# Kernel tuning notes

Measured on AMD Instinct MI355X. Metric: run time of the kernel, lower is better.

Reference implementation:

```python
import jax, jax.numpy as jnp
import numpy as np

N_NODES = 100000
N_EDGES = 1600000
DIMS = [128, 128, 40]   # embedding_dim
SS_DIM = 64
DROP_P = 0.2


def setup_inputs() -> dict:
    key = jax.random.key(0)
    ks = jax.random.split(key, 8)
    x = jax.random.normal(ks[0], (N_NODES, DIMS[0]), dtype=jnp.float32)
    adj_row = jax.random.randint(ks[1], (N_EDGES,), 0, N_NODES)
    adj_col = jax.random.randint(ks[2], (N_EDGES,), 0, N_NODES)
    adj_val = jax.random.uniform(ks[3], (N_EDGES,), dtype=jnp.float32)
    # nn.Linear(in, out, bias=False): y = x @ W.T; store transposed as (in, out)
    def lin(k, fi, fo):
        b = 1.0 / np.sqrt(fi)
        return jax.random.uniform(k, (fi, fo), minval=-b, maxval=b, dtype=jnp.float32)
    W0 = lin(ks[4], DIMS[0], DIMS[1])
    W1 = lin(ks[5], DIMS[1], DIMS[2])
    Wss = lin(ks[6], DIMS[-2], SS_DIM)
    return {"x": x, "adj_row": adj_row, "adj_col": adj_col, "adj_val": adj_val,
            "W0": W0, "W1": W1, "Wss": Wss}


def reference(x, adj_row, adj_col, adj_val, W0, W1, Wss):
    N = x.shape[0]
    keep = 1.0 - DROP_P

    def spmm(h):  # sparse [N,N] @ dense [N,d] via gather + segment_sum
        return jax.ops.segment_sum(adj_val[:, None] * h[adj_col], adj_row,
                                   num_segments=N)

    # deterministic dropout masks (fixed key, training path val_test=False)
    k1, k2 = jax.random.split(jax.random.key(42))
    m1 = jax.random.bernoulli(k1, keep, (N, W0.shape[1]))
    m2 = jax.random.bernoulli(k2, keep, (N, W0.shape[1]))

    # main branch: ln=0 -> spmm, lin0, relu, dropout; ln=1 -> spmm, lin1
    h = jnp.where(m1, jax.nn.relu(spmm(x) @ W0) / keep, 0.0)
    h = spmm(h) @ W1

    # self-supervised branch: ln=0 -> spmm, lin0, relu, dropout; ln=1 -> spmm; classifier
    s = jnp.where(m2, jax.nn.relu(spmm(x) @ W0) / keep, 0.0)
    s = spmm(s) @ Wss
    return (h, s)
```

## Files before the change

### kernel.cpp

```cpp
#include <hip/hip_runtime.h>
#include <stdint.h>


#define NN 100000
#define NE 1600000
#define D 128
#define NW 400000
#define ZC 104
#define DO1 40
#define DO2 64
#define OUT_S_OFF 4000000
#define KEEP_THR 6710886u
#define NB 49
#define CAP 36000
#define MASKB 3125
#define CONVB 25000

typedef unsigned int uint;
typedef __attribute__((ext_vector_type(4))) float f32x4;
typedef __attribute__((ext_vector_type(8))) short short8;
union U4S8 { uint4 u; short8 s; };

__device__ __forceinline__ float bflo(uint p) { return __uint_as_float(p << 16); }
__device__ __forceinline__ float bfhi(uint p) { return __uint_as_float(p & 0xffff0000u); }
__device__ __forceinline__ uint f2bf(float f) {
  uint u = __float_as_uint(f);
  return (u + 0x7fffu + ((u >> 16) & 1u)) >> 16;
}
__device__ __forceinline__ uint pack2(float lo, float hi) {
  return f2bf(lo) | (f2bf(hi) << 16);
}

__device__ __forceinline__ void tf2x32(uint k0, uint k1, uint x0, uint x1,
                                       uint& o0, uint& o1) {
  uint ks2 = k0 ^ k1 ^ 0x1BD11BDAu;
  x0 += k0; x1 += k1;
#define TFR(r) { x0 += x1; x1 = (x1 << (r)) | (x1 >> (32 - (r))); x1 ^= x0; }
  TFR(13) TFR(15) TFR(26) TFR(6)
  x0 += k1;  x1 += ks2 + 1u;
  TFR(17) TFR(29) TFR(16) TFR(24)
  x0 += ks2; x1 += k0 + 2u;
  TFR(13) TFR(15) TFR(26) TFR(6)
  x0 += k0;  x1 += k1 + 3u;
  TFR(17) TFR(29) TFR(16) TFR(24)
  x0 += k1;  x1 += ks2 + 4u;
  TFR(13) TFR(15) TFR(26) TFR(6)
  x0 += ks2; x1 += k0 + 5u;
#undef TFR
  o0 = x0; o1 = x1;
}

__global__ void prep_kernel(const float* __restrict__ x, uint* __restrict__ xb,
                            uint* __restrict__ m1, uint* __restrict__ m2,
                            const float* __restrict__ W0, const float* __restrict__ W1,
                            const float* __restrict__ Wss,
                            ushort* __restrict__ w0t, ushort* __restrict__ wcatT,
                            int* __restrict__ cursor) {
  int bid = blockIdx.x, tid = threadIdx.x;
  if (bid < CONVB) {
    if (bid == 0 && tid < NB) cursor[tid] = tid * CAP;
    int i = bid * 256 + tid;
    float2 v = ((const float2*)x)[i];
    xb[i] = pack2(v.x, v.y);
  } else if (bid < CONVB + MASKB) {
    int t = (bid - CONVB) * 256 + tid;
    uint a0, a1, b0, b1;
    tf2x32(0u, 42u, 0u, 0u, a0, a1);
    tf2x32(0u, 42u, 0u, 1u, b0, b1);
    bool second = (t >= NW);
    uint w  = second ? (uint)(t - NW) : (uint)t;
    uint k0 = second ? b0 : a0;
    uint k1 = second ? b1 : a1;
    uint base = w * 32u;
    uint word = 0u;
    for (int i = 0; i < 32; ++i) {
      uint o0, o1;
      tf2x32(k0, k1, 0u, base + (uint)i, o0, o1);
      word |= (uint)(((o0 ^ o1) >> 9) <= KEEP_THR) << i;
    }
    (second ? m2 : m1)[w] = word;
  } else {
    int idx = (bid - CONVB - MASKB) * 256 + tid;
    if (idx < 16384) {
      int c = idx >> 7, k = idx & 127;
      w0t[idx] = (ushort)f2bf(W0[k * D + c]);
    } else {
      int j = idx - 16384;
      int c = j >> 7, k = j & 127;
      float v = (c < 40) ? W1[k * DO1 + c] : ((c < 48) ? 0.f : Wss[k * DO2 + (c - 48)]);
      wcatT[j] = (ushort)f2bf(v);
    }
  }
}

__global__ void bin_kernel(const int* __restrict__ row, const int* __restrict__ col,
                           const float* __restrict__ val, int* __restrict__ cursor,
                           uint2* __restrict__ buck) {
  __shared__ int h[NB];
  __shared__ int base[NB];
  int tid = threadIdx.x;
  if (tid < NB) h[tid] = 0;
  __syncthreads();
  int e0 = blockIdx.x * 8192;
#pragma unroll 4
  for (int j = 0; j < 32; ++j) {
    int e = e0 + j * 256 + tid;
    if (e < NE) atomicAdd(&h[row[e] >> 11], 1);
  }
  __syncthreads();
  if (tid < NB) {
    int c = h[tid];
    base[tid] = c ? atomicAdd(&cursor[tid], c) : 0;
    h[tid] = 0;
  }
  __syncthreads();
#pragma unroll 4
  for (int j = 0; j < 32; ++j) {
    int e = e0 + j * 256 + tid;
    if (e < NE) {
      int r = row[e];
      int b = r >> 11;
      int k = atomicAdd(&h[b], 1);
      int idx = base[b] + k;
      int lim = (b + 1) * CAP;
      if (idx >= lim) idx = lim - 1;
      buck[idx] = make_uint2(((uint)(r & 2047) << 17) | (uint)col[e],
                             __float_as_uint(val[e]));
    }
  }
}

__global__ __launch_bounds__(1024) void csr_kernel(const uint2* __restrict__ buck,
                                                   const int* __restrict__ cursor,
                                                   int* __restrict__ ptr,
                                                   uint2* __restrict__ cv) {
  __shared__ int cnt[2048];
  __shared__ int sc[2048];
  __shared__ int cb[NB];
  int b = blockIdx.x, tid = threadIdx.x;
  if (tid < NB) cb[tid] = min(cursor[tid] - tid * CAP, CAP);
  int i0 = tid, i1 = tid + 1024;
  cnt[i0] = 0; cnt[i1] = 0;
  __syncthreads();
  int gbase = 0;
  for (int i = 0; i < b; ++i) gbase += cb[i];
  int n = cb[b];
  int src = b * CAP;
  for (int i = tid; i < n; i += 1024) atomicAdd(&cnt[buck[src + i].x >> 17], 1);
  __syncthreads();
  sc[i0] = cnt[i0]; sc[i1] = cnt[i1];
  __syncthreads();
  for (int off = 1; off < 2048; off <<= 1) {
    int v0 = (i0 >= off) ? sc[i0 - off] : 0;
    int v1 = (i1 >= off) ? sc[i1 - off] : 0;
    __syncthreads();
    sc[i0] += v0; sc[i1] += v1;
    __syncthreads();
  }
  int r0 = b * 2048;
  int s0 = sc[i0] - cnt[i0], s1 = sc[i1] - cnt[i1];
  if (r0 + i0 < NN) ptr[r0 + i0] = gbase + s0;
  if (r0 + i1 < NN) ptr[r0 + i1] = gbase + s1;
  if (b == 0 && tid == 0) ptr[NN] = NE;
  cnt[i0] = s0; cnt[i1] = s1;
  __syncthreads();
  for (int i = tid; i < n; i += 1024) {
    uint2 e = buck[src + i];
    int rl = e.x >> 17;
    int k = atomicAdd(&cnt[rl], 1);
    cv[gbase + k] = make_uint2(e.x & 0x1FFFFu, e.y);
  }
}

__global__ void spmm_x_kernel(const int* __restrict__ ptr, const uint2* __restrict__ cv,
                              const uint2* __restrict__ xb, uint2* __restrict__ t) {
  int r = blockIdx.x * 8 + (threadIdx.x >> 5);
  int k = threadIdx.x & 31;
  int s = ptr[r], e = ptr[r + 1];
  float a0 = 0.f, a1 = 0.f, a2 = 0.f, a3 = 0.f;
  int i = s;
  for (; i + 4 <= e; i += 4) {
    uint2 e0 = cv[i], e1 = cv[i + 1], e2 = cv[i + 2], e3 = cv[i + 3];
    uint2 p0 = xb[e0.x * 32 + k];
    uint2 p1 = xb[e1.x * 32 + k];
    uint2 p2 = xb[e2.x * 32 + k];
    uint2 p3 = xb[e3.x * 32 + k];
    float v0 = __uint_as_float(e0.y), v1 = __uint_as_float(e1.y);
    float v2 = __uint_as_float(e2.y), v3 = __uint_as_float(e3.y);
    a0 += v0 * bflo(p0.x); a1 += v0 * bfhi(p0.x);
    a2 += v0 * bflo(p0.y); a3 += v0 * bfhi(p0.y);
    a0 += v1 * bflo(p1.x); a1 += v1 * bfhi(p1.x);
    a2 += v1 * bflo(p1.y); a3 += v1 * bfhi(p1.y);
    a0 += v2 * bflo(p2.x); a1 += v2 * bfhi(p2.x);
    a2 += v2 * bflo(p2.y); a3 += v2 * bfhi(p2.y);
    a0 += v3 * bflo(p3.x); a1 += v3 * bfhi(p3.x);
    a2 += v3 * bflo(p3.y); a3 += v3 * bfhi(p3.y);
  }
  for (; i < e; ++i) {
    uint2 ev = cv[i];
    float v = __uint_as_float(ev.y);
    uint2 p = xb[ev.x * 32 + k];
    a0 += v * bflo(p.x); a1 += v * bfhi(p.x);
    a2 += v * bflo(p.y); a3 += v * bfhi(p.y);
  }
  t[r * 32 + k] = make_uint2(pack2(a0, a1), pack2(a2, a3));
}

#define SWZ(row, byte) ((row) * 256 + ((byte) ^ ((((row) >> 1) & 7) << 4)))
__global__ __launch_bounds__(512, 4) void pass_a_kernel(
    const uint* __restrict__ tb, const ushort* __restrict__ w0t,
    const ushort* __restrict__ wcatT,
    const uint* __restrict__ m1, const uint* __restrict__ m2,
    ushort* __restrict__ zz) {
  __shared__ __align__(16) char ldsb[69632];
  uint* mlds = (uint*)(ldsb + 65536);

  int t = threadIdx.x;
  int r0 = blockIdx.x * 128;
  int wid = t >> 6, l = t & 63, lc = l & 15, lk = l >> 4;

#pragma unroll
  for (int i = 0; i < 4; ++i) {
    int lin = i * 512 + t;
    int row = lin >> 4, seg = lin & 15;
    int gr = r0 + row;
    uint4 v = make_uint4(0, 0, 0, 0);
    if (gr < NN) v = ((const uint4*)(tb + (size_t)gr * 64))[seg];
    *(uint4*)&ldsb[SWZ(row, seg * 16)] = v;
    uint4 w = ((const uint4*)w0t)[lin];
    *(uint4*)&ldsb[32768 + SWZ(row, seg * 16)] = w;
  }
#pragma unroll
  for (int i = 0; i < 2; ++i) {
    int idx = t;
    int row = idx >> 2, word = idx & 3;
    int gr = r0 + row;
    uint v = 0;
    if (gr < NN) v = (i == 0 ? m1 : m2)[gr * 4 + word];
    mlds[i * 512 + idx] = v;
  }
  __syncthreads();

  short8 af[4];
#pragma unroll
  for (int s = 0; s < 4; ++s) {
    U4S8 tmp; tmp.u = *(uint4*)&ldsb[SWZ(16 * wid + lc, 64 * s + 16 * lk)];
    af[s] = tmp.s;
  }
  f32x4 acc[8];
#pragma unroll
  for (int n = 0; n < 8; ++n) acc[n] = (f32x4)(0.f);
#pragma unroll
  for (int n = 0; n < 8; ++n) {
#pragma unroll
    for (int s = 0; s < 4; ++s) {
      U4S8 tmp; tmp.u = *(uint4*)&ldsb[32768 + SWZ(16 * n + lc, 64 * s + 16 * lk)];
      acc[n] = __builtin_amdgcn_mfma_f32_16x16x32_bf16(af[s], tmp.s, acc[n], 0, 0, 0);
    }
  }
  __syncthreads();

#pragma unroll
  for (int reg = 0; reg < 4; ++reg) {
    int row = 16 * wid + 4 * lk + reg;
    uint4 w1q = *(uint4*)&mlds[row * 4];
    uint4 w2q = *(uint4*)&mlds[512 + row * 4];
    uint w1a[4] = {w1q.x, w1q.y, w1q.z, w1q.w};
    uint w2a[4] = {w2q.x, w2q.y, w2q.z, w2q.w};
#pragma unroll
    for (int n = 0; n < 8; ++n) {
      float v = fmaxf(acc[n][reg], 0.f) * 1.25f;
      ushort ub = (ushort)f2bf(v);
      int bit = (n & 1) * 16 + lc;
      ushort u1 = ((w1a[n >> 1] >> bit) & 1u) ? ub : (ushort)0;
      ushort u2 = ((w2a[n >> 1] >> bit) & 1u) ? ub : (ushort)0;
      int ad = SWZ(row, 32 * n + 2 * lc);
      *(ushort*)&ldsb[ad] = u1;
      *(ushort*)&ldsb[32768 + ad] = u2;
    }
  }
  __syncthreads();

  f32x4 acc2[7];
#pragma unroll
  for (int n = 0; n < 7; ++n) acc2[n] = (f32x4)(0.f);
#pragma unroll
  for (int n2 = 0; n2 < 7; ++n2) {
    int ubase = (n2 < 3) ? 0 : 32768;
#pragma unroll
    for (int s = 0; s < 4; ++s) {
      U4S8 a2; a2.u = ((const uint4*)wcatT)[(16 * n2 + lc) * 16 + 4 * s + lk];
      U4S8 b2; b2.u = *(uint4*)&ldsb[ubase + SWZ(16 * wid + lc, 64 * s + 16 * lk)];
      acc2[n2] = __builtin_amdgcn_mfma_f32_16x16x32_bf16(a2.s, b2.s, acc2[n2], 0, 0, 0);
    }
  }

  int r = r0 + 16 * wid + lc;
  if (r < NN) {
#pragma unroll
    for (int n2 = 0; n2 < 7; ++n2) {
      if (n2 == 2 && lk >= 2) continue;
      int cb = 16 * n2 + 4 * lk;
      if (n2 >= 3) cb -= 8;
      uint2 v = make_uint2(pack2(acc2[n2][0], acc2[n2][1]),
                           pack2(acc2[n2][2], acc2[n2][3]));
      *(uint2*)(zz + (size_t)r * ZC + cb) = v;
    }
  }
}

__global__ void gather_out_kernel(const int* __restrict__ ptr, const uint2* __restrict__ cv,
                                  const uint2* __restrict__ zp, float* __restrict__ out) {
  int r = blockIdx.x * 8 + (threadIdx.x >> 5);
  int k = threadIdx.x & 31;
  if (k >= 26) return;
  int s = ptr[r], e = ptr[r + 1];
  float a0 = 0.f, a1 = 0.f, a2 = 0.f, a3 = 0.f;
  int i = s;
  for (; i + 4 <= e; i += 4) {
    uint2 e0 = cv[i], e1 = cv[i + 1], e2 = cv[i + 2], e3 = cv[i + 3];
    uint2 p0 = zp[e0.x * 26 + k];
    uint2 p1 = zp[e1.x * 26 + k];
    uint2 p2 = zp[e2.x * 26 + k];
    uint2 p3 = zp[e3.x * 26 + k];
    float v0 = __uint_as_float(e0.y), v1 = __uint_as_float(e1.y);
    float v2 = __uint_as_float(e2.y), v3 = __uint_as_float(e3.y);
    a0 += v0 * bflo(p0.x); a1 += v0 * bfhi(p0.x);
    a2 += v0 * bflo(p0.y); a3 += v0 * bfhi(p0.y);
    a0 += v1 * bflo(p1.x); a1 += v1 * bfhi(p1.x);
    a2 += v1 * bflo(p1.y); a3 += v1 * bfhi(p1.y);
    a0 += v2 * bflo(p2.x); a1 += v2 * bfhi(p2.x);
    a2 += v2 * bflo(p2.y); a3 += v2 * bfhi(p2.y);
    a0 += v3 * bflo(p3.x); a1 += v3 * bfhi(p3.x);
    a2 += v3 * bflo(p3.y); a3 += v3 * bfhi(p3.y);
  }
  for (; i < e; ++i) {
    uint2 ev = cv[i];
    float v = __uint_as_float(ev.y);
    uint2 p = zp[ev.x * 26 + k];
    a0 += v * bflo(p.x); a1 += v * bfhi(p.x);
    a2 += v * bflo(p.y); a3 += v * bfhi(p.y);
  }
  if (k < 10) {
    *(float4*)(out + (size_t)r * DO1 + 4 * k) = make_float4(a0, a1, a2, a3);
  } else {
    *(float4*)(out + OUT_S_OFF + (size_t)r * DO2 + 4 * (k - 10)) = make_float4(a0, a1, a2, a3);
  }
}

extern "C" void kernel_launch(void* const* d_in, const int* in_sizes, int n_in,
                              void* d_out, int out_size, void* d_ws, size_t ws_size,
                              hipStream_t stream) {
  const float* x       = (const float*)d_in[0];
  const int*   adj_row = (const int*)d_in[1];
  const int*   adj_col = (const int*)d_in[2];
  const float* adj_val = (const float*)d_in[3];
  const float* W0      = (const float*)d_in[4];
  const float* W1      = (const float*)d_in[5];
  const float* Wss     = (const float*)d_in[6];
  float* out = (float*)d_out;

  char* ws = (char*)d_ws;
  uint*   t_bf  = (uint*)(ws + 0);
  uint2*  buck  = (uint2*)(ws + 0);
  uint*   xb    = (uint*)(ws + 25600000);
  ushort* zz    = (ushort*)(ws + 25600000);
  uint*   m1    = (uint*)(ws + 51200000);
  uint*   m2    = (uint*)(ws + 52800000);
  int*    ptr   = (int*)(ws + 54400000);
  ushort* w0t   = (ushort*)(ws + 54800016);
  ushort* wcatT = (ushort*)(ws + 54832784);
  int*    curs  = (int*)(ws + 54861456);
  uint2*  cv    = (uint2*)(ws + 55600016);

  prep_kernel<<<CONVB + MASKB + 120, 256, 0, stream>>>(x, xb, m1, m2, W0, W1, Wss,
                                                       w0t, wcatT, curs);
  bin_kernel<<<196, 256, 0, stream>>>(adj_row, adj_col, adj_val, curs, buck);
  csr_kernel<<<NB, 1024, 0, stream>>>(buck, curs, ptr, cv);
  spmm_x_kernel<<<12500, 256, 0, stream>>>(ptr, cv, (const uint2*)xb, (uint2*)t_bf);
  pass_a_kernel<<<782, 512, 0, stream>>>(t_bf, w0t, wcatT, m1, m2, zz);
  gather_out_kernel<<<12500, 256, 0, stream>>>(ptr, cv, (const uint2*)zz, out);
}
```

Before: 308.9 us.

## Fuse binning with conversion and mask generation with CSR build

Merges edge binning into the x/weight conversion kernel and moves dropout mask generation into the CSR build kernel. Cursor initialization becomes a memset with relative offsets. The x-to-bf16 conversion is widened to float4 per thread. The goal is fewer kernel launches and letting independent work fill idle CUs during the small-grid bin and CSR phases. In exchange there is an extra memset launch and a heavier, mixed-role block dispatch.

```diff
diff --git a/kernel.cpp b/kernel.cpp
--- a/kernel.cpp
+++ b/kernel.cpp
@@ -13,8 +13,10 @@
 #define KEEP_THR 6710886u
 #define NB 49
 #define CAP 36000
-#define MASKB 3125
-#define CONVB 25000
+#define BINB 196
+#define CONVB 12500
+#define CSRB 49
+#define MASKB1K 782
 
 typedef unsigned int uint;
 typedef __attribute__((ext_vector_type(4))) float f32x4;
@@ -50,20 +52,72 @@
   o0 = x0; o1 = x1;
 }
 
-__global__ void prep_kernel(const float* __restrict__ x, uint* __restrict__ xb,
-                            uint* __restrict__ m1, uint* __restrict__ m2,
-                            const float* __restrict__ W0, const float* __restrict__ W1,
-                            const float* __restrict__ Wss,
-                            ushort* __restrict__ w0t, ushort* __restrict__ wcatT,
-                            int* __restrict__ cursor) {
+__global__ void bin_conv_kernel(const int* __restrict__ row, const int* __restrict__ col,
+                                const float* __restrict__ val, int* __restrict__ cursor,
+                                uint2* __restrict__ buck,
+                                const float* __restrict__ x, uint* __restrict__ xb,
+                                const float* __restrict__ W0, const float* __restrict__ W1,
+                                const float* __restrict__ Wss,
+                                ushort* __restrict__ w0t, ushort* __restrict__ wcatT) {
   int bid = blockIdx.x, tid = threadIdx.x;
-  if (bid < CONVB) {
-    if (bid == 0 && tid < NB) cursor[tid] = tid * CAP;
-    int i = bid * 256 + tid;
-    float2 v = ((const float2*)x)[i];
-    xb[i] = pack2(v.x, v.y);
-  } else if (bid < CONVB + MASKB) {
-    int t = (bid - CONVB) * 256 + tid;
+  if (bid < BINB) {
+    __shared__ int h[NB];
+    __shared__ int base[NB];
+    if (tid < NB) h[tid] = 0;
+    __syncthreads();
+    int e0 = bid * 8192;
+#pragma unroll 4
+    for (int j = 0; j < 32; ++j) {
+      int e = e0 + j * 256 + tid;
+      if (e < NE) atomicAdd(&h[row[e] >> 11], 1);
+    }
+    __syncthreads();
+    if (tid < NB) {
+      int c = h[tid];
+      base[tid] = c ? (tid * CAP + atomicAdd(&cursor[tid], c)) : 0;
+      h[tid] = 0;
+    }
+    __syncthreads();
+#pragma unroll 4
+    for (int j = 0; j < 32; ++j) {
+      int e = e0 + j * 256 + tid;
+      if (e < NE) {
+        int r = row[e];
+        int b = r >> 11;
+        int k = atomicAdd(&h[b], 1);
+        int idx = base[b] + k;
+        int lim = (b + 1) * CAP;
+        if (idx >= lim) idx = lim - 1;
+        buck[idx] = make_uint2(((uint)(r & 2047) << 17) | (uint)col[e],
+                               __float_as_uint(val[e]));
+      }
+    }
+  } else if (bid < BINB + CONVB) {
+    int i = (bid - BINB) * 256 + tid;
+    float4 v = ((const float4*)x)[i];
+    ((uint2*)xb)[i] = make_uint2(pack2(v.x, v.y), pack2(v.z, v.w));
+  } else {
+    int idx = (bid - BINB - CONVB) * 256 + tid;
+    if (idx < 16384) {
+      int c = idx >> 7, k = idx & 127;
+      w0t[idx] = (ushort)f2bf(W0[k * D + c]);
+    } else {
+      int j = idx - 16384;
+      int c = j >> 7, k = j & 127;
+      float v = (c < 40) ? W1[k * DO1 + c] : ((c < 48) ? 0.f : Wss[k * DO2 + (c - 48)]);
+      wcatT[j] = (ushort)f2bf(v);
+    }
+  }
+}
+
+__global__ __launch_bounds__(1024) void csr_mask_kernel(
+    const uint2* __restrict__ buck, const int* __restrict__ cursor,
+    int* __restrict__ ptr, uint2* __restrict__ cv,
+    uint* __restrict__ m1, uint* __restrict__ m2) {
+  int bid = blockIdx.x, tid = threadIdx.x;
+  if (bid >= CSRB) {
+    int t = (bid - CSRB) * 1024 + tid;
+    if (t >= 2 * NW) return;
     uint a0, a1, b0, b1;
     tf2x32(0u, 42u, 0u, 0u, a0, a1);
     tf2x32(0u, 42u, 0u, 1u, b0, b1);
@@ -79,66 +133,13 @@
       word |= (uint)(((o0 ^ o1) >> 9) <= KEEP_THR) << i;
     }
     (second ? m2 : m1)[w] = word;
-  } else {
-    int idx = (bid - CONVB - MASKB) * 256 + tid;
-    if (idx < 16384) {
-      int c = idx >> 7, k = idx & 127;
-      w0t[idx] = (ushort)f2bf(W0[k * D + c]);
-    } else {
-      int j = idx - 16384;
-      int c = j >> 7, k = j & 127;
-      float v = (c < 40) ? W1[k * DO1 + c] : ((c < 48) ? 0.f : Wss[k * DO2 + (c - 48)]);
-      wcatT[j] = (ushort)f2bf(v);
-    }
-  }
-}
-
-__global__ void bin_kernel(const int* __restrict__ row, const int* __restrict__ col,
-                           const float* __restrict__ val, int* __restrict__ cursor,
-                           uint2* __restrict__ buck) {
-  __shared__ int h[NB];
-  __shared__ int base[NB];
-  int tid = threadIdx.x;
-  if (tid < NB) h[tid] = 0;
-  __syncthreads();
-  int e0 = blockIdx.x * 8192;
-#pragma unroll 4
-  for (int j = 0; j < 32; ++j) {
-    int e = e0 + j * 256 + tid;
-    if (e < NE) atomicAdd(&h[row[e] >> 11], 1);
-  }
-  __syncthreads();
-  if (tid < NB) {
-    int c = h[tid];
-    base[tid] = c ? atomicAdd(&cursor[tid], c) : 0;
-    h[tid] = 0;
-  }
-  __syncthreads();
-#pragma unroll 4
-  for (int j = 0; j < 32; ++j) {
-    int e = e0 + j * 256 + tid;
-    if (e < NE) {
-      int r = row[e];
-      int b = r >> 11;
-      int k = atomicAdd(&h[b], 1);
-      int idx = base[b] + k;
-      int lim = (b + 1) * CAP;
-      if (idx >= lim) idx = lim - 1;
-      buck[idx] = make_uint2(((uint)(r & 2047) << 17) | (uint)col[e],
-                             __float_as_uint(val[e]));
-    }
-  }
-}
-
-__global__ __launch_bounds__(1024) void csr_kernel(const uint2* __restrict__ buck,
-                                                   const int* __restrict__ cursor,
-                                                   int* __restrict__ ptr,
-                                                   uint2* __restrict__ cv) {
+    return;
+  }
   __shared__ int cnt[2048];
   __shared__ int sc[2048];
   __shared__ int cb[NB];
-  int b = blockIdx.x, tid = threadIdx.x;
-  if (tid < NB) cb[tid] = min(cursor[tid] - tid * CAP, CAP);
+  int b = bid;
+  if (tid < NB) cb[tid] = min(cursor[tid], CAP);
   int i0 = tid, i1 = tid + 1024;
   cnt[i0] = 0; cnt[i1] = 0;
   __syncthreads();
@@ -373,10 +374,10 @@
   int*    curs  = (int*)(ws + 54861456);
   uint2*  cv    = (uint2*)(ws + 55600016);
 
-  prep_kernel<<<CONVB + MASKB + 120, 256, 0, stream>>>(x, xb, m1, m2, W0, W1, Wss,
-                                                       w0t, wcatT, curs);
-  bin_kernel<<<196, 256, 0, stream>>>(adj_row, adj_col, adj_val, curs, buck);
-  csr_kernel<<<NB, 1024, 0, stream>>>(buck, curs, ptr, cv);
+  hipMemsetAsync(curs, 0, NB * sizeof(int), stream);
+  bin_conv_kernel<<<BINB + CONVB + 120, 256, 0, stream>>>(
+      adj_row, adj_col, adj_val, curs, buck, x, xb, W0, W1, Wss, w0t, wcatT);
+  csr_mask_kernel<<<CSRB + MASKB1K, 1024, 0, stream>>>(buck, curs, ptr, cv, m1, m2);
   spmm_x_kernel<<<12500, 256, 0, stream>>>(ptr, cv, (const uint2*)xb, (uint2*)t_bf);
   pass_a_kernel<<<782, 512, 0, stream>>>(t_bf, w0t, wcatT, m1, m2, zz);
   gather_out_kernel<<<12500, 256, 0, stream>>>(ptr, cv, (const uint2*)zz, out);
```

Result: faster. 282.7 us (-8.5%).
